# Optimization experiments

Measured on AMD Instinct MI355X. Metric: run time of the kernel, lower is better.

Reference implementation:

```python
import jax, jax.numpy as jnp
from jax import lax
import numpy as np

N, I, H, B, T = 16, 128, 128, 32, 512  # n lstms, input_size, hidden_size, batch, seq_len


def setup_inputs() -> dict:
    key = jax.random.key(0)
    k0, k1, k2, k3, k4 = jax.random.split(key, 5)
    s = 1.0 / np.sqrt(H)  # PyTorch LSTM init scale U(-1/sqrt(H), 1/sqrt(H)); normal*s is fine numerically
    x = jax.random.normal(k0, (B, T, N * I), dtype=jnp.float32)
    W_ih = jax.random.normal(k1, (N, 4 * H, I), dtype=jnp.float32) * s
    W_hh = jax.random.normal(k2, (N, 4 * H, H), dtype=jnp.float32) * s
    b_ih = jax.random.normal(k3, (N, 4 * H), dtype=jnp.float32) * s
    b_hh = jax.random.normal(k4, (N, 4 * H), dtype=jnp.float32) * s
    return {"x": x, "W_ih": W_ih, "W_hh": W_hh, "b_ih": b_ih, "b_hh": b_hh}


def reference(x, W_ih, W_hh, b_ih, b_hh):
    """WideLSTM fused forward: N independent single-layer unidirectional LSTMs,
    hx=None (zero initial state), batch_first output [B, T, N*H], (h_n, c_n) [1, B, N*H].
    PyTorch gate order: i, f, g, o."""
    Bx, Tx, _ = x.shape
    n = W_ih.shape[0]
    h = W_hh.shape[-1]
    xs = x.reshape(Bx, Tx, n, -1).transpose(1, 0, 2, 3)  # [T, B, N, I]
    # Precompute input contribution + biases for all timesteps at once (one big GEMM)
    x_proj = jnp.einsum('tbni,ngi->tbng', xs, W_ih) + (b_ih + b_hh)  # [T, B, N, 4H]

    def step(carry, xp):
        hprev, cprev = carry
        z = xp + jnp.einsum('bnh,ngh->bng', hprev, W_hh)  # [B, N, 4H]
        i_g, f_g, g_g, o_g = jnp.split(z, 4, axis=-1)
        i_g = jax.nn.sigmoid(i_g)
        f_g = jax.nn.sigmoid(f_g)
        g_g = jnp.tanh(g_g)
        o_g = jax.nn.sigmoid(o_g)
        c = f_g * cprev + i_g * g_g
        hnew = o_g * jnp.tanh(c)
        return (hnew, c), hnew

    h0 = jnp.zeros((Bx, n, h), dtype=x.dtype)
    c0 = jnp.zeros((Bx, n, h), dtype=x.dtype)
    (h_n, c_n), hs = lax.scan(step, (h0, c0), x_proj)
    output = hs.transpose(1, 0, 2, 3).reshape(Bx, Tx, n * h)  # [B, T, N*H]
    h_n = h_n.reshape(1, Bx, n * h)  # [num_layers*num_dir=1, B, N*H]
    c_n = c_n.reshape(1, Bx, n * h)
    return output, h_n, c_n
```

## Files before the change

kernel.cpp:

```cpp
#include <hip/hip_runtime.h>

#define N_LSTM 16
#define ISZ 128
#define HSZ 128
#define BSZ 32
#define TSZ 512
#define G4H 512
#define XROW (N_LSTM * ISZ)
#define OROW (N_LSTM * HSZ)

typedef __attribute__((ext_vector_type(8))) short s16x8;
typedef __attribute__((ext_vector_type(4))) float f32x4;

static __device__ __forceinline__ unsigned short f2bf(float f) {
    unsigned int u = __builtin_bit_cast(unsigned int, f);
    u += 0x7fffu + ((u >> 16) & 1u);
    return (unsigned short)(u >> 16);
}

static __device__ __forceinline__ float fast_sigmoid(float x) {
    float e = __expf(-x);
    return __builtin_amdgcn_rcpf(1.0f + e);
}

static __device__ __forceinline__ float fast_tanh(float x) {
    x = fminf(fmaxf(x, -20.0f), 20.0f);
    float e = __expf(-2.0f * x);
    return (1.0f - e) * __builtin_amdgcn_rcpf(1.0f + e);
}

static __device__ __forceinline__ void barrier_lgkm() {
    __builtin_amdgcn_sched_barrier(0);
    asm volatile("s_waitcnt lgkmcnt(0)" ::: "memory");
    __builtin_amdgcn_s_barrier();
    __builtin_amdgcn_sched_barrier(0);
}

__global__ __launch_bounds__(512, 2) void widelstm_fused(
    const float* __restrict__ x, const float* __restrict__ Wih,
    const float* __restrict__ Whh, const float* __restrict__ bih,
    const float* __restrict__ bhh, float* __restrict__ out)
{
    __shared__ __align__(16) unsigned short xbuf[2][16][136];
    __shared__ __align__(16) unsigned short hbuf[2][16][136];

    const int tid = threadIdx.x;
    const int wv  = tid >> 6;
    const int ln  = tid & 63;
    const int lm  = ln & 15;
    const int lq  = ln >> 4;
    const int n    = blockIdx.x >> 1;
    const int half = blockIdx.x & 1;
    const int b0   = half * 16;

    s16x8 wih[4][4], whh[4][4];
    float bias[4];
    #pragma unroll
    for (int g = 0; g < 4; ++g) {
        const int col = g * 128 + wv * 16 + lm;
        bias[g] = bih[n * G4H + col] + bhh[n * G4H + col];
        #pragma unroll
        for (int kt = 0; kt < 4; ++kt) {
            const float* pi = Wih + ((size_t)n * G4H + col) * ISZ + kt * 32 + lq * 8;
            const float* ph = Whh + ((size_t)n * G4H + col) * HSZ + kt * 32 + lq * 8;
            s16x8 a, b;
            #pragma unroll
            for (int j = 0; j < 8; ++j) {
                a[j] = (short)f2bf(pi[j]);
                b[j] = (short)f2bf(ph[j]);
            }
            wih[g][kt] = a;
            whh[g][kt] = b;
        }
    }

    for (int i = tid; i < 16 * 136; i += 512)
        ((unsigned short*)hbuf[0])[i] = 0;

    const int sr = tid >> 5;
    const int sc = (tid & 31) * 4;
    const float* xrow = x + (size_t)(b0 + sr) * TSZ * XROW + n * ISZ + sc;

    float4 xr = *(const float4*)(xrow);
    {
        unsigned int lo = (unsigned int)f2bf(xr.x) | ((unsigned int)f2bf(xr.y) << 16);
        unsigned int hi = (unsigned int)f2bf(xr.z) | ((unsigned int)f2bf(xr.w) << 16);
        *(uint2*)&xbuf[0][sr][sc] = make_uint2(lo, hi);
    }
    barrier_lgkm();

    f32x4 xacc[4];
    #pragma unroll
    for (int g = 0; g < 4; ++g)
        xacc[g] = (f32x4){bias[g], bias[g], bias[g], bias[g]};
    #pragma unroll
    for (int kt = 0; kt < 4; ++kt) {
        s16x8 axk = *(const s16x8*)&xbuf[0][lm][kt * 32 + lq * 8];
        #pragma unroll
        for (int g = 0; g < 4; ++g)
            xacc[g] = __builtin_amdgcn_mfma_f32_16x16x32_bf16(axk, wih[g][kt], xacc[g], 0, 0, 0);
    }

    xr = *(const float4*)(xrow + (size_t)XROW);

    float cprev[4] = {0.f, 0.f, 0.f, 0.f};
    float hlast[4] = {0.f, 0.f, 0.f, 0.f};
    const int ocol = n * HSZ + wv * 16 + lm;

#define LSTM_STEP(T_, CUR_, NXT_)                                                          \
    {                                                                                      \
        const int t_ = (T_);                                                               \
        if (t_ + 1 < TSZ) {                                                                \
            unsigned int lo = (unsigned int)f2bf(xr.x) | ((unsigned int)f2bf(xr.y) << 16); \
            unsigned int hi = (unsigned int)f2bf(xr.z) | ((unsigned int)f2bf(xr.w) << 16); \
            *(uint2*)&xbuf[NXT_][sr][sc] = make_uint2(lo, hi);                             \
        }                                                                                  \
        barrier_lgkm();                    \
        s16x8 ah0 = *(const s16x8*)&hbuf[CUR_][lm][0 * 32 + lq * 8];                       \
        s16x8 ah1 = *(const s16x8*)&hbuf[CUR_][lm][1 * 32 + lq * 8];                       \
        s16x8 ah2 = *(const s16x8*)&hbuf[CUR_][lm][2 * 32 + lq * 8];                       \
        s16x8 ah3 = *(const s16x8*)&hbuf[CUR_][lm][3 * 32 + lq * 8];                       \
        if (t_ + 2 < TSZ)                                                                  \
            xr = *(const float4*)(xrow + (size_t)(t_ + 2) * XROW);                         \
        f32x4 hacc[4];                                                                     \
        _Pragma("unroll")                                                                  \
        for (int g = 0; g < 4; ++g)                                                        \
            hacc[g] = __builtin_amdgcn_mfma_f32_16x16x32_bf16(ah0, whh[g][0], xacc[g], 0, 0, 0); \
        _Pragma("unroll")                                                                  \
        for (int g = 0; g < 4; ++g)                                                        \
            hacc[g] = __builtin_amdgcn_mfma_f32_16x16x32_bf16(ah1, whh[g][1], hacc[g], 0, 0, 0); \
        _Pragma("unroll")                                                                  \
        for (int g = 0; g < 4; ++g)                                                        \
            hacc[g] = __builtin_amdgcn_mfma_f32_16x16x32_bf16(ah2, whh[g][2], hacc[g], 0, 0, 0); \
        _Pragma("unroll")                                                                  \
        for (int g = 0; g < 4; ++g)                                                        \
            hacc[g] = __builtin_amdgcn_mfma_f32_16x16x32_bf16(ah3, whh[g][3], hacc[g], 0, 0, 0); \
        if (t_ + 1 < TSZ) {               \
            _Pragma("unroll")                                                              \
            for (int g = 0; g < 4; ++g)                                                    \
                xacc[g] = (f32x4){bias[g], bias[g], bias[g], bias[g]};                     \
            _Pragma("unroll")                                                              \
            for (int kt = 0; kt < 4; ++kt) {                                               \
                s16x8 axk = *(const s16x8*)&xbuf[NXT_][lm][kt * 32 + lq * 8];              \
                _Pragma("unroll")                                                          \
                for (int g = 0; g < 4; ++g)                                                \
                    xacc[g] = __builtin_amdgcn_mfma_f32_16x16x32_bf16(axk, wih[g][kt], xacc[g], 0, 0, 0); \
            }                                                                              \
        }                                                                                  \
        float* orow = out + (size_t)t_ * OROW + ocol;                                      \
        _Pragma("unroll")                                                                  \
        for (int r = 0; r < 4; ++r) {                                                      \
            float iv = fast_sigmoid(hacc[0][r]);                                           \
            float fv = fast_sigmoid(hacc[1][r]);                                           \
            float gv = fast_tanh(hacc[2][r]);                                              \
            float ov = fast_sigmoid(hacc[3][r]);                                           \
            float c  = fv * cprev[r] + iv * gv;                                            \
            cprev[r] = c;                                                                  \
            float hv = ov * fast_tanh(c);                                                  \
            hlast[r] = hv;                                                                 \
            const int row = lq * 4 + r;                                                    \
            orow[(size_t)(b0 + row) * TSZ * OROW] = hv;                                    \
            hbuf[NXT_][row][wv * 16 + lm] = f2bf(hv);                                      \
        }                                                                                  \
    }

    for (int t = 0; t < TSZ; t += 2) {
        LSTM_STEP(t, 0, 1);
        LSTM_STEP(t + 1, 1, 0);
    }
#undef LSTM_STEP

    const size_t hn_off = (size_t)BSZ * TSZ * OROW;
    const size_t cn_off = hn_off + (size_t)BSZ * OROW;
    #pragma unroll
    for (int r = 0; r < 4; ++r) {
        const int row = lq * 4 + r;
        const size_t idx = (size_t)(b0 + row) * OROW + ocol;
        out[hn_off + idx] = hlast[r];
        out[cn_off + idx] = cprev[r];
    }
}

extern "C" void kernel_launch(void* const* d_in, const int* in_sizes, int n_in,
                              void* d_out, int out_size, void* d_ws, size_t ws_size,
                              hipStream_t stream) {
    const float* x   = (const float*)d_in[0];
    const float* Wih = (const float*)d_in[1];
    const float* Whh = (const float*)d_in[2];
    const float* bih = (const float*)d_in[3];
    const float* bhh = (const float*)d_in[4];
    float* out = (float*)d_out;
    widelstm_fused<<<dim3(32), dim3(512), 0, stream>>>(x, Wih, Whh, bih, bhh, out);
}
```

Before: 782.8 us.

## Pre-convert input to bf16 in a separate pass and fuse gate reciprocals

Adds a pre-pass kernel that converts x to bf16 and writes it into the workspace in the exact per-block, per-thread layout the recurrent kernel reads. Each step then loads a contiguous 8-byte chunk instead of a strided float4 and skips the conversion. The gate math is also rearranged to merge two reciprocals into one (i*g and o*tanh(c)), and output pointers are precomputed and advanced each step. The cost is an extra kernel launch and a full pass over x, which only pays off if the strided x loads were on the critical path of the serial loop.

```diff
diff --git a/kernel.cpp b/kernel.cpp
--- a/kernel.cpp
+++ b/kernel.cpp
@@ -18,17 +18,6 @@
     return (unsigned short)(u >> 16);
 }
 
-static __device__ __forceinline__ float fast_sigmoid(float x) {
-    float e = __expf(-x);
-    return __builtin_amdgcn_rcpf(1.0f + e);
-}
-
-static __device__ __forceinline__ float fast_tanh(float x) {
-    x = fminf(fmaxf(x, -20.0f), 20.0f);
-    float e = __expf(-2.0f * x);
-    return (1.0f - e) * __builtin_amdgcn_rcpf(1.0f + e);
-}
-
 static __device__ __forceinline__ void barrier_lgkm() {
     __builtin_amdgcn_sched_barrier(0);
     asm volatile("s_waitcnt lgkmcnt(0)" ::: "memory");
@@ -36,10 +25,31 @@
     __builtin_amdgcn_sched_barrier(0);
 }
 
+__global__ void x_to_bf16(const float* __restrict__ x,
+                          unsigned long long* __restrict__ xbf) {
+    const int G = blockIdx.x * 256 + threadIdx.x;
+    const int tid = G & 511;
+    const int wg  = (G >> 9) & 31;
+    const int t   = G >> 14;
+    const int sr = tid >> 5;
+    const int sc = (tid & 31) * 4;
+    const int n  = wg >> 1;
+    const int b0 = (wg & 1) * 16;
+    const float* src = x + (size_t)(b0 + sr) * (TSZ * XROW) + (size_t)t * XROW + n * ISZ + sc;
+    float4 v = *(const float4*)src;
+    unsigned long long r = (unsigned long long)f2bf(v.x)
+                         | ((unsigned long long)f2bf(v.y) << 16)
+                         | ((unsigned long long)f2bf(v.z) << 32)
+                         | ((unsigned long long)f2bf(v.w) << 48);
+    xbf[G] = r;
+}
+
+template <int PRE>
 __global__ __launch_bounds__(512, 2) void widelstm_fused(
-    const float* __restrict__ x, const float* __restrict__ Wih,
-    const float* __restrict__ Whh, const float* __restrict__ bih,
-    const float* __restrict__ bhh, float* __restrict__ out)
+    const float* __restrict__ x, const unsigned long long* __restrict__ xbf,
+    const float* __restrict__ Wih, const float* __restrict__ Whh,
+    const float* __restrict__ bih, const float* __restrict__ bhh,
+    float* __restrict__ out)
 {
     __shared__ __align__(16) unsigned short xbuf[2][16][136];
     __shared__ __align__(16) unsigned short hbuf[2][16][136];
@@ -80,9 +90,15 @@
     const int sr = tid >> 5;
     const int sc = (tid & 31) * 4;
     const float* xrow = x + (size_t)(b0 + sr) * TSZ * XROW + n * ISZ + sc;
-
-    float4 xr = *(const float4*)(xrow);
-    {
+    const unsigned long long* xbase = xbf + (size_t)blockIdx.x * 512 + tid;
+
+    float4 xr;
+    uint2  xr2;
+    if constexpr (PRE) {
+        xr2 = *(const uint2*)xbase;
+        *(uint2*)&xbuf[0][sr][sc] = xr2;
+    } else {
+        xr = *(const float4*)(xrow);
         unsigned int lo = (unsigned int)f2bf(xr.x) | ((unsigned int)f2bf(xr.y) << 16);
         unsigned int hi = (unsigned int)f2bf(xr.z) | ((unsigned int)f2bf(xr.w) << 16);
         *(uint2*)&xbuf[0][sr][sc] = make_uint2(lo, hi);
@@ -101,27 +117,40 @@
             xacc[g] = __builtin_amdgcn_mfma_f32_16x16x32_bf16(axk, wih[g][kt], xacc[g], 0, 0, 0);
     }
 
-    xr = *(const float4*)(xrow + (size_t)XROW);
+    if constexpr (PRE) xr2 = *(const uint2*)(xbase + 16384);
+    else               xr  = *(const float4*)(xrow + (size_t)XROW);
+    const unsigned long long* xptr = xbase + 2 * 16384;
 
     float cprev[4] = {0.f, 0.f, 0.f, 0.f};
     float hlast[4] = {0.f, 0.f, 0.f, 0.f};
     const int ocol = n * HSZ + wv * 16 + lm;
+
+    float* po0 = out + (size_t)(b0 + lq * 4 + 0) * TSZ * OROW + ocol;
+    float* po1 = out + (size_t)(b0 + lq * 4 + 1) * TSZ * OROW + ocol;
+    float* po2 = out + (size_t)(b0 + lq * 4 + 2) * TSZ * OROW + ocol;
+    float* po3 = out + (size_t)(b0 + lq * 4 + 3) * TSZ * OROW + ocol;
 
 #define LSTM_STEP(T_, CUR_, NXT_)                                                          \
     {                                                                                      \
         const int t_ = (T_);                                                               \
         if (t_ + 1 < TSZ) {                                                                \
-            unsigned int lo = (unsigned int)f2bf(xr.x) | ((unsigned int)f2bf(xr.y) << 16); \
-            unsigned int hi = (unsigned int)f2bf(xr.z) | ((unsigned int)f2bf(xr.w) << 16); \
-            *(uint2*)&xbuf[NXT_][sr][sc] = make_uint2(lo, hi);                             \
+            if constexpr (PRE) {                                                           \
+                *(uint2*)&xbuf[NXT_][sr][sc] = xr2;                                        \
+            } else {                                                                       \
+                unsigned int lo = (unsigned int)f2bf(xr.x) | ((unsigned int)f2bf(xr.y) << 16); \
+                unsigned int hi = (unsigned int)f2bf(xr.z) | ((unsigned int)f2bf(xr.w) << 16); \
+                *(uint2*)&xbuf[NXT_][sr][sc] = make_uint2(lo, hi);                         \
+            }                                                                              \
         }                                                                                  \
         barrier_lgkm();                    \
         s16x8 ah0 = *(const s16x8*)&hbuf[CUR_][lm][0 * 32 + lq * 8];                       \
         s16x8 ah1 = *(const s16x8*)&hbuf[CUR_][lm][1 * 32 + lq * 8];                       \
         s16x8 ah2 = *(const s16x8*)&hbuf[CUR_][lm][2 * 32 + lq * 8];                       \
         s16x8 ah3 = *(const s16x8*)&hbuf[CUR_][lm][3 * 32 + lq * 8];                       \
-        if (t_ + 2 < TSZ)                                                                  \
-            xr = *(const float4*)(xrow + (size_t)(t_ + 2) * XROW);                         \
+        if (t_ + 2 < TSZ) {                                                                \
+            if constexpr (PRE) { xr2 = *(const uint2*)xptr; xptr += 16384; }               \
+            else               { xr = *(const float4*)(xrow + (size_t)(t_ + 2) * XROW); }  \
+        }                                                                                  \
         f32x4 hacc[4];                                                                     \
         _Pragma("unroll")                                                                  \
         for (int g = 0; g < 4; ++g)                                                        \
@@ -147,20 +176,28 @@
                     xacc[g] = __builtin_amdgcn_mfma_f32_16x16x32_bf16(axk, wih[g][kt], xacc[g], 0, 0, 0); \
             }                                                                              \
         }                                                                                  \
-        float* orow = out + (size_t)t_ * OROW + ocol;                                      \
+                 \
         _Pragma("unroll")                                                                  \
         for (int r = 0; r < 4; ++r) {                                                      \
-            float iv = fast_sigmoid(hacc[0][r]);                                           \
-            float fv = fast_sigmoid(hacc[1][r]);                                           \
-            float gv = fast_tanh(hacc[2][r]);                                              \
-            float ov = fast_sigmoid(hacc[3][r]);                                           \
-            float c  = fv * cprev[r] + iv * gv;                                            \
-            cprev[r] = c;                                                                  \
-            float hv = ov * fast_tanh(c);                                                  \
-            hlast[r] = hv;                                                                 \
-            const int row = lq * 4 + r;                                                    \
-            orow[(size_t)(b0 + row) * TSZ * OROW] = hv;                                    \
-            hbuf[NXT_][row][wv * 16 + lm] = f2bf(hv);                                      \
+            float zi = hacc[0][r], zf = hacc[1][r], zg = hacc[2][r], zo = hacc[3][r];      \
+            float ei = __expf(-zi);                                                        \
+            float ef = __expf(-zf);                                                        \
+            float eo = __expf(-zo);                                                        \
+            float zgc = fminf(fmaxf(zg, -20.f), 20.f);                                     \
+            float eg  = __expf(-2.f * zgc);                                                \
+            float fv  = __builtin_amdgcn_rcpf(1.f + ef);                                   \
+            float ig  = (1.f - eg) * __builtin_amdgcn_rcpf((1.f + ei) * (1.f + eg));       \
+            float c   = fv * cprev[r] + ig;                                                \
+            cprev[r]  = c;                                                                 \
+            float cc  = fminf(fmaxf(c, -20.f), 20.f);                                      \
+            float ec  = __expf(-2.f * cc);                                                 \
+            float hv  = (1.f - ec) * __builtin_amdgcn_rcpf((1.f + eo) * (1.f + ec));       \
+            hlast[r]  = hv;                                                                \
+            hbuf[NXT_][lq * 4 + r][wv * 16 + lm] = f2bf(hv);                               \
+            if (r == 0) { *po0 = hv; po0 += OROW; }                                        \
+            if (r == 1) { *po1 = hv; po1 += OROW; }                                        \
+            if (r == 2) { *po2 = hv; po2 += OROW; }                                        \
+            if (r == 3) { *po3 = hv; po3 += OROW; }                                        \
         }                                                                                  \
     }
 
@@ -190,5 +227,13 @@
     const float* bih = (const float*)d_in[3];
     const float* bhh = (const float*)d_in[4];
     float* out = (float*)d_out;
-    widelstm_fused<<<dim3(32), dim3(512), 0, stream>>>(x, Wih, Whh, bih, bhh, out);
-}
+
+    const size_t need = (size_t)TSZ * 32 * 512 * 8;
+    if (d_ws != nullptr && ws_size >= need) {
+        unsigned long long* xbf = (unsigned long long*)d_ws;
+        x_to_bf16<<<dim3(32768), dim3(256), 0, stream>>>(x, xbf);
+        widelstm_fused<1><<<dim3(32), dim3(512), 0, stream>>>(x, xbf, Wih, Whh, bih, bhh, out);
+    } else {
+        widelstm_fused<0><<<dim3(32), dim3(512), 0, stream>>>(x, nullptr, Wih, Whh, bih, bhh, out);
+    }
+}
```

Result: no change. 790.3 us (+1.0%).
